# Performance work log

Measured on AMD Instinct MI355X. Metric: run time of the kernel, lower is better.

Reference implementation:

```python
import jax, jax.numpy as jnp
import numpy as np

N, C, K, OUT = 16384, 64, 32, 64
EPS = 1e-5


def knn_idx(x, k):
    # pairwise squared distances, exclude self-loops, take k nearest
    sq = jnp.sum(x * x, axis=1)
    d = sq[:, None] + sq[None, :] - 2.0 * (x @ x.T)  # [N, N]
    n = x.shape[0]
    d = d.at[jnp.arange(n), jnp.arange(n)].set(jnp.inf)
    _, idx = jax.lax.top_k(-d, k)  # [N, k] nearest neighbors
    return idx


def edge_conv(x, idx, W, b, g, beta):
    # EdgeConv: max_j nn(cat([x_i, x_j - x_i])), nn = Lin -> ReLU -> BN
    xi = jnp.broadcast_to(x[:, None, :], (x.shape[0], idx.shape[1], x.shape[1]))
    xj = x[idx]                                   # [N, k, C] gather
    e = jnp.concatenate([xi, xj - xi], axis=-1)   # [N, k, 2C]
    h = jax.nn.relu(e @ W + b)                    # [N, k, H]
    mu = h.mean(axis=(0, 1))
    var = h.var(axis=(0, 1))
    h = (h - mu) * jax.lax.rsqrt(var + EPS) * g + beta  # BN (batch stats)
    return h.max(axis=1)                          # max aggregation over k


def setup_inputs() -> dict:
    key = jax.random.key(0)
    ks = jax.random.split(key, 14)
    s = 0.05
    H = 2 * C
    return {
        "x": jax.random.normal(ks[0], (N, C), dtype=jnp.float32),
        "W1": jax.random.normal(ks[1], (2 * C, H), dtype=jnp.float32) * s,
        "b1": jnp.zeros((H,), jnp.float32),
        "g1": jnp.ones((H,), jnp.float32),
        "beta1": jnp.zeros((H,), jnp.float32),
        "W2": jax.random.normal(ks[2], (2 * H, H), dtype=jnp.float32) * s,
        "b2": jnp.zeros((H,), jnp.float32),
        "g2": jnp.ones((H,), jnp.float32),
        "beta2": jnp.zeros((H,), jnp.float32),
        "lw1": jax.random.normal(ks[3], (H, C), dtype=jnp.float32) * s,
        "lb1": jnp.zeros((C,), jnp.float32),
        "lw2": jax.random.normal(ks[4], (C, OUT), dtype=jnp.float32) * s,
        "lb2": jnp.zeros((OUT,), jnp.float32),
    }


def reference(x, W1, b1, g1, beta1, W2, b2, g2, beta2, lw1, lb1, lw2, lb2):
    idx1 = knn_idx(x, K)
    h1 = edge_conv(x, idx1, W1, b1, g1, beta1)    # [N, 2C]
    idx2 = knn_idx(h1, K)                          # dynamic graph in feature space
    h2 = edge_conv(h1, idx2, W2, b2, g2, beta2)   # [N, 2C]
    h = jax.nn.relu(h2)
    h = jax.nn.relu(h @ lw1 + lb1)                # [N, C]
    return h @ lw2 + lb2                          # [N, OUT]
```

## Files before the change

### kernel.cpp

```cpp
#include <hip/hip_runtime.h>
#include <hip/hip_bf16.h>
#include <math.h>

#define N_PTS 16384
#define KNN_K 32
#define CAP 512
#define HDIM 128
#define TSAMP 4096
#define NSLICE 4
#define LBUF 64

typedef __attribute__((ext_vector_type(8))) short bf16x8;
typedef __attribute__((ext_vector_type(8))) unsigned short us8;
typedef __attribute__((ext_vector_type(4))) float f32x4;

template<int C>
__global__ void sqnorm_np_kernel(const float* __restrict__ feat, float* __restrict__ sq) {
  int r = blockIdx.x * 256 + threadIdx.x;
  if (r >= N_PTS) return;
  const float* xr = feat + (size_t)r * C;
  float acc[8];
  #pragma unroll
  for (int j = 0; j < 8; j++) acc[j] = __fmul_rn(xr[j], xr[j]);
  for (int i = 8; i < C; i += 8) {
    #pragma unroll
    for (int j = 0; j < 8; j++)
      acc[j] = __fadd_rn(acc[j], __fmul_rn(xr[i + j], xr[i + j]));
  }
  float s01 = __fadd_rn(acc[0], acc[1]);
  float s23 = __fadd_rn(acc[2], acc[3]);
  float s45 = __fadd_rn(acc[4], acc[5]);
  float s67 = __fadd_rn(acc[6], acc[7]);
  sq[r] = __fadd_rn(__fadd_rn(s01, s23), __fadd_rn(s45, s67));
}

template<int C>
__global__ void split_swz_kernel(const float* __restrict__ x, unsigned short* __restrict__ hi,
                                 unsigned short* __restrict__ lo) {
  constexpr int CH = C / 8;
  int gid = blockIdx.x * 256 + threadIdx.x;
  int n = gid / CH, c = gid & (CH - 1);
  if (n >= N_PTS) return;
  const float* src = x + (size_t)n * C + c * 8;
  unsigned short h8[8], l8[8];
  #pragma unroll
  for (int j = 0; j < 8; j++) {
    float v = src[j];
    __hip_bfloat16 h = __float2bfloat16(v);
    float hf = __bfloat162float(h);
    __hip_bfloat16 l = __float2bfloat16(v - hf);
    h8[j] = *(unsigned short*)&h;
    l8[j] = *(unsigned short*)&l;
  }
  size_t o = (size_t)n * C + (size_t)(((c ^ (n & (CH - 1)))) * 8);
  *(us8*)(hi + o) = *(const us8*)h8;
  *(us8*)(lo + o) = *(const us8*)l8;
}

template<int C>
__launch_bounds__(512)
__global__ void knn_tau(const unsigned short* __restrict__ xhi,
                        const unsigned short* __restrict__ xlo,
                        const float* __restrict__ sq,
                        float margin, float* __restrict__ tau) {
  constexpr int CH = C / 8, KC = C / 32;
  constexpr int NB = 32 * C * 2;
  constexpr int SEGS = (2 * NB) / 16 / 512;
  __shared__ unsigned char Bs[2 * NB];
  __shared__ float tred[64][65];
  const int t = threadIdx.x;
  const int qbase = blockIdx.x * 64;
  const int wv = t >> 6, lane = t & 63, qd = lane >> 4, l16 = lane & 15;
  const int mi = (wv & 3) * 16, ni = (wv >> 2) * 16;

  bf16x8 ah[KC], al[KC];
  {
    const int arow = qbase + mi + l16;
    const int akey = arow & (CH - 1);
    #pragma unroll
    for (int kc = 0; kc < KC; kc++) {
      size_t o = (size_t)arow * C + (size_t)(((kc * 4 + qd) ^ akey) * 8);
      ah[kc] = *(const bf16x8*)(xhi + o);
      al[kc] = *(const bf16x8*)(xlo + o);
    }
  }
  int qr[4];
  #pragma unroll
  for (int r = 0; r < 4; r++) qr[r] = qbase + mi + qd * 4 + r;
  float t0[4], t1[4];
  #pragma unroll
  for (int r = 0; r < 4; r++) { t0[r] = INFINITY; t1[r] = INFINITY; }

  const int brow = ni + l16;
  const int bkey = brow & (CH - 1);

  us8 regs[SEGS];
  #pragma unroll
  for (int s = 0; s < SEGS; s++) {
    int boff = (t + s * 512) * 16;
    int mtx = boff >= NB;
    int off = boff & (NB - 1);
    regs[s] = *(const us8*)((mtx ? xlo : xhi) + off / 2);
  }
  for (int ti = 0; ti < TSAMP / 32; ti++) {
    __syncthreads();
    #pragma unroll
    for (int s = 0; s < SEGS; s++) {
      int boff = (t + s * 512) * 16;
      int mtx = boff >= NB;
      int off = boff & (NB - 1);
      *(us8*)&Bs[mtx * NB + off] = regs[s];
    }
    __syncthreads();
    if (ti + 1 < TSAMP / 32) {
      #pragma unroll
      for (int s = 0; s < SEGS; s++) {
        int boff = (t + s * 512) * 16;
        int mtx = boff >= NB;
        int off = boff & (NB - 1);
        regs[s] = *(const us8*)((mtx ? xlo : xhi) + (size_t)(ti + 1) * 32 * C + off / 2);
      }
    }
    f32x4 acc = {0.f, 0.f, 0.f, 0.f};
    #pragma unroll
    for (int kc = 0; kc < KC; kc++) {
      size_t bo = (size_t)brow * (2 * C) + (size_t)(((kc * 4 + qd) ^ bkey) * 16);
      bf16x8 bh = *(const bf16x8*)&Bs[bo];
      bf16x8 bl = *(const bf16x8*)&Bs[NB + bo];
      acc = __builtin_amdgcn_mfma_f32_16x16x32_bf16(ah[kc], bh, acc, 0, 0, 0);
      acc = __builtin_amdgcn_mfma_f32_16x16x32_bf16(ah[kc], bl, acc, 0, 0, 0);
      acc = __builtin_amdgcn_mfma_f32_16x16x32_bf16(al[kc], bh, acc, 0, 0, 0);
    }
    const int j = ti * 32 + ni + l16;
    const float sj = sq[j];
    #pragma unroll
    for (int r = 0; r < 4; r++) {
      float d = fmaf(-2.f, acc[r], sj);
      if (d < t1[r] && j != qr[r]) {
        bool lt = d < t0[r];
        t1[r] = lt ? t0[r] : d;
        t0[r] = lt ? d : t0[r];
      }
    }
  }
  const int strm = ni + l16;
  #pragma unroll
  for (int r = 0; r < 4; r++) {
    tred[mi + qd * 4 + r][strm]      = t0[r];
    tred[mi + qd * 4 + r][32 + strm] = t1[r];
  }
  __syncthreads();
  const int tq = t >> 3, i0 = (t & 7) * 8;
  #pragma unroll
  for (int ii = 0; ii < 8; ii++) {
    const int i = i0 + ii;
    const float vi = tred[tq][i];
    int rank = 0;
    for (int m = 0; m < 64; m++) {
      float vm = tred[tq][m];
      rank += (vm < vi || (vm == vi && m < i)) ? 1 : 0;
    }
    if (rank == 32) tau[qbase + tq] = vi + margin;
  }
}

template<int C>
__launch_bounds__(512)
__global__ void knn_filter(const unsigned short* __restrict__ xhi,
                           const unsigned short* __restrict__ xlo,
                           const float* __restrict__ sq,
                           const float* __restrict__ tau,
                           int* __restrict__ cnt, int* __restrict__ list_j,
                           float* __restrict__ list_d) {
  constexpr int CH = C / 8, KC = C / 32;
  constexpr int NB = 32 * C * 2;
  constexpr int SEGS = (2 * NB) / 16 / 512;
  constexpr int JSPAN = N_PTS / NSLICE;
  __shared__ unsigned char Bs[2 * NB];
  __shared__ int   lbj[64 * LBUF];
  __shared__ float lbd[64 * LBUF];
  __shared__ int lcnt[64];
  __shared__ int lbase[64];
  const int t = threadIdx.x;
  const int qbase = blockIdx.x * 64;
  const int jbase = blockIdx.y * JSPAN;
  const int wv = t >> 6, lane = t & 63, qd = lane >> 4, l16 = lane & 15;
  const int mi = (wv & 3) * 16, ni = (wv >> 2) * 16;

  if (t < 64) lcnt[t] = 0;

  bf16x8 ah[KC], al[KC];
  {
    const int arow = qbase + mi + l16;
    const int akey = arow & (CH - 1);
    #pragma unroll
    for (int kc = 0; kc < KC; kc++) {
      size_t o = (size_t)arow * C + (size_t)(((kc * 4 + qd) ^ akey) * 8);
      ah[kc] = *(const bf16x8*)(xhi + o);
      al[kc] = *(const bf16x8*)(xlo + o);
    }
  }
  int lq[4]; float tq[4];
  #pragma unroll
  for (int r = 0; r < 4; r++) {
    lq[r] = mi + qd * 4 + r;
    tq[r] = tau[qbase + lq[r]];
  }
  const int brow = ni + l16;
  const int bkey = brow & (CH - 1);

  us8 regs[SEGS];
  #pragma unroll
  for (int s = 0; s < SEGS; s++) {
    int boff = (t + s * 512) * 16;
    int mtx = boff >= NB;
    int off = boff & (NB - 1);
    regs[s] = *(const us8*)((mtx ? xlo : xhi) + (size_t)jbase * C + off / 2);
  }
  for (int ti = 0; ti < JSPAN / 32; ti++) {
    __syncthreads();
    #pragma unroll
    for (int s = 0; s < SEGS; s++) {
      int boff = (t + s * 512) * 16;
      int mtx = boff >= NB;
      int off = boff & (NB - 1);
      *(us8*)&Bs[mtx * NB + off] = regs[s];
    }
    __syncthreads();
    if (ti + 1 < JSPAN / 32) {
      #pragma unroll
      for (int s = 0; s < SEGS; s++) {
        int boff = (t + s * 512) * 16;
        int mtx = boff >= NB;
        int off = boff & (NB - 1);
        regs[s] = *(const us8*)((mtx ? xlo : xhi) + (size_t)(jbase + (ti + 1) * 32) * C + off / 2);
      }
    }
    f32x4 acc = {0.f, 0.f, 0.f, 0.f};
    #pragma unroll
    for (int kc = 0; kc < KC; kc++) {
      size_t bo = (size_t)brow * (2 * C) + (size_t)(((kc * 4 + qd) ^ bkey) * 16);
      bf16x8 bh = *(const bf16x8*)&Bs[bo];
      bf16x8 bl = *(const bf16x8*)&Bs[NB + bo];
      acc = __builtin_amdgcn_mfma_f32_16x16x32_bf16(ah[kc], bh, acc, 0, 0, 0);
      acc = __builtin_amdgcn_mfma_f32_16x16x32_bf16(ah[kc], bl, acc, 0, 0, 0);
      acc = __builtin_amdgcn_mfma_f32_16x16x32_bf16(al[kc], bh, acc, 0, 0, 0);
    }
    const int j = jbase + ti * 32 + ni + l16;
    const float sj = sq[j];
    #pragma unroll
    for (int r = 0; r < 4; r++) {
      float d = fmaf(-2.f, acc[r], sj);
      if (d <= tq[r] && j != qbase + lq[r]) {
        int pos = atomicAdd(&lcnt[lq[r]], 1);
        if (pos < LBUF) {
          lbj[lq[r] * LBUF + pos] = j;
          lbd[lq[r] * LBUF + pos] = d;
        } else {
          int gp = atomicAdd(&cnt[qbase + lq[r]], 1);
          if (gp < CAP) {
            list_j[(size_t)(qbase + lq[r]) * CAP + gp] = j;
            list_d[(size_t)(qbase + lq[r]) * CAP + gp] = d;
          }
        }
      }
    }
  }
  __syncthreads();
  if (t < 64) {
    int c = lcnt[t]; if (c > LBUF) c = LBUF;
    lcnt[t] = c;
    lbase[t] = atomicAdd(&cnt[qbase + t], c);
  }
  __syncthreads();
  for (int v = t; v < 64 * LBUF; v += 512) {
    int q = v / LBUF, e = v % LBUF;
    if (e < lcnt[q]) {
      int p = lbase[q] + e;
      if (p < CAP) {
        list_j[(size_t)(qbase + q) * CAP + p] = lbj[v];
        list_d[(size_t)(qbase + q) * CAP + p] = lbd[v];
      }
    }
  }
}

__global__ void zero_cnt_kernel(int* __restrict__ cnt) {
  cnt[blockIdx.x * 256 + threadIdx.x] = 0;
}

template<int C>
__launch_bounds__(256)
__global__ void knn_refine_np(const float* __restrict__ feat, const float* __restrict__ sq,
                              const int* __restrict__ cnt, const int* __restrict__ list_j,
                              const float* __restrict__ list_d, float wmarg,
                              int* __restrict__ idx_out) {
  __shared__ float ds[CAP];
  __shared__ int   js[CAP];
  __shared__ int   widx[CAP];
  __shared__ float dnp[CAP];
  __shared__ float xqs[C];
  __shared__ float rows[32 * (C + 1)];
  __shared__ int   jl[32];
  __shared__ float sjl[32];
  __shared__ float cutd;
  __shared__ int   wn;
  const int q = blockIdx.x;
  const int t = threadIdx.x;
  for (int v = t; v < C; v += 256) xqs[v] = feat[(size_t)q * C + v];
  int cq = cnt[q]; if (cq > CAP) cq = CAP;
  const float sqq = sq[q];
  if (t == 0) { wn = 0; cutd = INFINITY; }
  for (int e = t; e < cq; e += 256) {
    js[e] = list_j[(size_t)q * CAP + e];
    ds[e] = list_d[(size_t)q * CAP + e];
  }
  __syncthreads();
  if (cq > KNN_K) {
    for (int e = t; e < cq; e += 256) {
      float d = ds[e]; int j = js[e];
      int rank = 0;
      for (int m = 0; m < cq; m++) {
        float dm = ds[m]; int jm = js[m];
        rank += (dm < d || (dm == d && jm < j)) ? 1 : 0;
      }
      if (rank == KNN_K - 1) cutd = d;
    }
  }
  __syncthreads();
  const float wcut = cutd + wmarg;
  for (int e = t; e < cq; e += 256)
    if (ds[e] <= wcut) { int p = atomicAdd(&wn, 1); widx[p] = e; }
  __syncthreads();
  const int nw = wn;
  for (int base = 0; base < nw; base += 32) {
    const int nc = (nw - base < 32) ? (nw - base) : 32;
    __syncthreads();
    if (t < nc) {
      int j = js[widx[base + t]];
      jl[t] = j;
      sjl[t] = sq[j];
    }
    __syncthreads();
    for (int v = t; v < nc * C; v += 256) {
      int r = v >> ((C == 64) ? 6 : 7);
      int c = v & (C - 1);
      rows[r * (C + 1) + c] = feat[(size_t)jl[r] * C + c];
    }
    __syncthreads();
    if (t < nc) {
      float g = 0.f;
      const float* row = &rows[t * (C + 1)];
      for (int c = 0; c < C; c++) g = fmaf(xqs[c], row[c], g);
      dnp[base + t] = __fsub_rn(__fadd_rn(sqq, sjl[t]), __fmul_rn(2.f, g));
    }
  }
  __syncthreads();
  for (int e = t; e < nw; e += 256) {
    float d = dnp[e]; int j = js[widx[e]];
    int rank = 0;
    for (int m = 0; m < nw; m++) {
      float dm = dnp[m]; int jm = js[widx[m]];
      rank += (dm < d || (dm == d && jm < j)) ? 1 : 0;
    }
    if (rank < KNN_K) idx_out[(size_t)q * KNN_K + rank] = j;
  }
}

template<int C>
__global__ void pq_kernel(const float* __restrict__ feat, const float* __restrict__ W,
                          const float* __restrict__ b, float* __restrict__ P,
                          float* __restrict__ Q) {
  int gid = blockIdx.x * 256 + threadIdx.x;
  int n = gid >> 7, ch = gid & 127;
  const float* xr = feat + (size_t)n * C;
  double p = (double)b[ch], q = 0.0;
  for (int d = 0; d < C; d++) {
    double xv = (double)xr[d];
    p += xv * (double)W[(size_t)d * HDIM + ch];
    q += xv * (double)W[(size_t)(C + d) * HDIM + ch];
  }
  P[gid] = (float)(p - q);
  Q[gid] = (float)q;
}

__global__ void edge_gather2(const float* __restrict__ P, const float* __restrict__ Q,
                             const int* __restrict__ idx, float* __restrict__ hmax,
                             float* __restrict__ hmin, double* __restrict__ stats) {
  __shared__ double red0[256];
  __shared__ double red1[256];
  const int t = threadIdx.x;
  const int ch = t & 127, half = t >> 7;
  const size_t nb = (size_t)blockIdx.x * 16 + (size_t)half * 8;
  double s = 0.0, s2 = 0.0;
  for (int u = 0; u < 8; u++) {
    const size_t n = nb + u;
    double p = (double)P[n * 128 + ch];
    double mx = -1.0e300, mn = 1.0e300;
    for (int k = 0; k < KNN_K; k++) {
      int j = idx[n * KNN_K + k];
      double h = p + (double)Q[(size_t)j * 128 + ch];
      h = h > 0.0 ? h : 0.0;
      mx = h > mx ? h : mx;
      mn = h < mn ? h : mn;
      s += h; s2 += h * h;
    }
    hmax[n * 128 + ch] = (float)mx;
    hmin[n * 128 + ch] = (float)mn;
  }
  red0[t] = s; red1[t] = s2;
  __syncthreads();
  if (t < 128) {
    atomicAdd(&stats[ch],       red0[t] + red0[t + 128]);
    atomicAdd(&stats[128 + ch], red1[t] + red1[t + 128]);
  }
}

__global__ void zero_stats_d(double* __restrict__ stats) {
  stats[threadIdx.x] = 0.0;
}

__global__ void bn_finalize_d(const double* __restrict__ stats, const float* __restrict__ g,
                              const float* __restrict__ beta, double* __restrict__ ss) {
  int ch = threadIdx.x;
  const double inv = 1.0 / ((double)N_PTS * (double)KNN_K);
  double mu = stats[ch] * inv;
  double var = stats[128 + ch] * inv - mu * mu;
  double sc = (double)g[ch] / sqrt(var + 1e-5);
  ss[ch] = sc;
  ss[128 + ch] = (double)beta[ch] - mu * sc;
}

__global__ void ec_out_d(const float* __restrict__ hmax, const float* __restrict__ hmin,
                         const double* __restrict__ ss, float* __restrict__ h_f) {
  size_t i = (size_t)blockIdx.x * 256 + threadIdx.x;
  int ch = (int)(i & 127);
  double sc = ss[ch];
  double v = sc >= 0.0 ? (double)hmax[i] : (double)hmin[i];
  h_f[i] = (float)(v * sc + ss[128 + ch]);
}

__global__ void head1_kernel(const float* __restrict__ h2, const float* __restrict__ lw1,
                             const float* __restrict__ lb1, float* __restrict__ T) {
  int gid = blockIdx.x * 256 + threadIdx.x;
  int n = gid >> 6, hc = gid & 63;
  const float* hr = h2 + (size_t)n * 128;
  double a = (double)lb1[hc];
  for (int d = 0; d < 128; d++) {
    double v = (double)hr[d];
    v = v > 0.0 ? v : 0.0;
    a += v * (double)lw1[(size_t)d * 64 + hc];
  }
  T[gid] = (float)(a > 0.0 ? a : 0.0);
}

__global__ void head2_kernel(const float* __restrict__ T, const float* __restrict__ lw2,
                             const float* __restrict__ lb2, float* __restrict__ out) {
  int gid = blockIdx.x * 256 + threadIdx.x;
  int n = gid >> 6, oc = gid & 63;
  const float* tr = T + (size_t)n * 64;
  double a = (double)lb2[oc];
  for (int d = 0; d < 64; d++) a += (double)tr[d] * (double)lw2[(size_t)d * 64 + oc];
  out[gid] = (float)a;
}

extern "C" void kernel_launch(void* const* d_in, const int* in_sizes, int n_in,
                              void* d_out, int out_size, void* d_ws, size_t ws_size,
                              hipStream_t stream) {
  (void)in_sizes; (void)n_in; (void)out_size; (void)ws_size;
  const float* x     = (const float*)d_in[0];
  const float* W1    = (const float*)d_in[1];
  const float* b1    = (const float*)d_in[2];
  const float* g1    = (const float*)d_in[3];
  const float* beta1 = (const float*)d_in[4];
  const float* W2    = (const float*)d_in[5];
  const float* b2    = (const float*)d_in[6];
  const float* g2    = (const float*)d_in[7];
  const float* beta2 = (const float*)d_in[8];
  const float* lw1   = (const float*)d_in[9];
  const float* lb1   = (const float*)d_in[10];
  const float* lw2   = (const float*)d_in[11];
  const float* lb2   = (const float*)d_in[12];
  float* out = (float*)d_out;

  char* w = (char*)d_ws;
  size_t off = 0;
  auto alloc = [&](size_t bytes) { char* p = w + off; off += (bytes + 255) & ~(size_t)255; return p; };
  float*  sq     = (float*) alloc(N_PTS * 4);
  float*  tau    = (float*) alloc(N_PTS * 4);
  int*    cnt    = (int*)   alloc(N_PTS * 4);
  int*    list_j = (int*)   alloc((size_t)N_PTS * CAP * 4);
  float*  list_d = (float*) alloc((size_t)N_PTS * CAP * 4);
  int*    idx    = (int*)   alloc((size_t)N_PTS * KNN_K * 4);
  unsigned short* xhi = (unsigned short*)alloc((size_t)N_PTS * HDIM * 2);
  unsigned short* xlo = (unsigned short*)alloc((size_t)N_PTS * HDIM * 2);
  float*  P      = (float*) alloc((size_t)N_PTS * HDIM * 4);
  float*  Q      = (float*) alloc((size_t)N_PTS * HDIM * 4);
  float*  hmax   = (float*) alloc((size_t)N_PTS * HDIM * 4);
  float*  hmin   = (float*) alloc((size_t)N_PTS * HDIM * 4);
  double* stats  = (double*)alloc(2 * HDIM * 8);
  double* ss     = (double*)alloc(2 * HDIM * 8);
  float*  h1f    = (float*) alloc((size_t)N_PTS * HDIM * 4);
  float*  h2f    = P;
  float*  T      = Q;

  sqnorm_np_kernel<64><<<N_PTS / 256, 256, 0, stream>>>(x, sq);
  split_swz_kernel<64><<<N_PTS * 8 / 256, 256, 0, stream>>>(x, xhi, xlo);
  knn_tau<64><<<N_PTS / 64, 512, 0, stream>>>(xhi, xlo, sq, 0.05f, tau);
  zero_cnt_kernel<<<N_PTS / 256, 256, 0, stream>>>(cnt);
  knn_filter<64><<<dim3(N_PTS / 64, NSLICE), 512, 0, stream>>>(xhi, xlo, sq, tau, cnt, list_j, list_d);
  knn_refine_np<64><<<N_PTS, 256, 0, stream>>>(x, sq, cnt, list_j, list_d, 0.05f, idx);

  pq_kernel<64><<<N_PTS * 128 / 256, 256, 0, stream>>>(x, W1, b1, P, Q);
  zero_stats_d<<<1, 256, 0, stream>>>(stats);
  edge_gather2<<<N_PTS / 16, 256, 0, stream>>>(P, Q, idx, hmax, hmin, stats);
  bn_finalize_d<<<1, 128, 0, stream>>>(stats, g1, beta1, ss);
  ec_out_d<<<N_PTS * HDIM / 256, 256, 0, stream>>>(hmax, hmin, ss, h1f);

  sqnorm_np_kernel<128><<<N_PTS / 256, 256, 0, stream>>>(h1f, sq);
  split_swz_kernel<128><<<N_PTS * 16 / 256, 256, 0, stream>>>(h1f, xhi, xlo);
  knn_tau<128><<<N_PTS / 64, 512, 0, stream>>>(xhi, xlo, sq, 0.2f, tau);
  zero_cnt_kernel<<<N_PTS / 256, 256, 0, stream>>>(cnt);
  knn_filter<128><<<dim3(N_PTS / 64, NSLICE), 512, 0, stream>>>(xhi, xlo, sq, tau, cnt, list_j, list_d);
  knn_refine_np<128><<<N_PTS, 256, 0, stream>>>(h1f, sq, cnt, list_j, list_d, 0.2f, idx);

  pq_kernel<128><<<N_PTS * 128 / 256, 256, 0, stream>>>(h1f, W2, b2, P, Q);
  zero_stats_d<<<1, 256, 0, stream>>>(stats);
  edge_gather2<<<N_PTS / 16, 256, 0, stream>>>(P, Q, idx, hmax, hmin, stats);
  bn_finalize_d<<<1, 128, 0, stream>>>(stats, g2, beta2, ss);
  ec_out_d<<<N_PTS * HDIM / 256, 256, 0, stream>>>(hmax, hmin, ss, h2f);

  head1_kernel<<<N_PTS * 64 / 256, 256, 0, stream>>>(h2f, lw1, lb1, T);
  head2_kernel<<<N_PTS * 64 / 256, 256, 0, stream>>>(T, lw2, lb2, out);
}
```

Before: 1.331 ms.

## Retile kNN filter to 128x64 tiles with 32x32 MFMA and split hi/lo staging

The kNN distance filter kernel now processes 128 queries per block against 64-point candidate tiles using 32x32x16 bf16 MFMA instead of 16x16x32. The hi and lo bf16 halves of the candidate tile are staged through a single shared buffer in two phases, which halves the shared memory footprint and doubles per-block query reuse of each loaded tile. The aim is to cut global/LDS traffic per distance and raise MFMA efficiency, at the cost of extra barriers per tile, 16 threshold registers per lane, and a smaller per-query local candidate buffer (48 entries) that spills to global atomics more often. Launch bounds now request 4 waves/SIMD occupancy.

```diff
diff --git a/kernel.cpp b/kernel.cpp
--- a/kernel.cpp
+++ b/kernel.cpp
@@ -8,11 +8,12 @@
 #define HDIM 128
 #define TSAMP 4096
 #define NSLICE 4
-#define LBUF 64
+#define LBUF 48
 
 typedef __attribute__((ext_vector_type(8))) short bf16x8;
 typedef __attribute__((ext_vector_type(8))) unsigned short us8;
 typedef __attribute__((ext_vector_type(4))) float f32x4;
+typedef __attribute__((ext_vector_type(16))) float f32x16;
 
 template<int C>
 __global__ void sqnorm_np_kernel(const float* __restrict__ feat, float* __restrict__ sq) {
@@ -165,115 +166,123 @@
 }
 
 template<int C>
-__launch_bounds__(512)
+__launch_bounds__(512, 4)
 __global__ void knn_filter(const unsigned short* __restrict__ xhi,
                            const unsigned short* __restrict__ xlo,
                            const float* __restrict__ sq,
                            const float* __restrict__ tau,
                            int* __restrict__ cnt, int* __restrict__ list_j,
                            float* __restrict__ list_d) {
-  constexpr int CH = C / 8, KC = C / 32;
-  constexpr int NB = 32 * C * 2;
-  constexpr int SEGS = (2 * NB) / 16 / 512;
+  constexpr int CH = C / 8;
+  constexpr int KC = C / 16;
+  constexpr int NB = 64 * C;
+  constexpr int SEGS = (NB * 2) / 16 / 512;
   constexpr int JSPAN = N_PTS / NSLICE;
-  __shared__ unsigned char Bs[2 * NB];
-  __shared__ int   lbj[64 * LBUF];
-  __shared__ float lbd[64 * LBUF];
-  __shared__ int lcnt[64];
-  __shared__ int lbase[64];
+  __shared__ unsigned short Bs[NB];
+  __shared__ int   lbj[128 * LBUF];
+  __shared__ float lbd[128 * LBUF];
+  __shared__ int lcnt[128];
+  __shared__ int lbase[128];
   const int t = threadIdx.x;
-  const int qbase = blockIdx.x * 64;
+  const int qbase = blockIdx.x * 128;
   const int jbase = blockIdx.y * JSPAN;
-  const int wv = t >> 6, lane = t & 63, qd = lane >> 4, l16 = lane & 15;
-  const int mi = (wv & 3) * 16, ni = (wv >> 2) * 16;
-
-  if (t < 64) lcnt[t] = 0;
+  const int wv = t >> 6, lane = t & 63;
+  const int l32 = lane & 31, hk = lane >> 5;
+  const int mi = (wv & 3) * 32, ni = (wv >> 2) * 32;
+
+  if (t < 128) lcnt[t] = 0;
 
   bf16x8 ah[KC], al[KC];
   {
-    const int arow = qbase + mi + l16;
+    const int arow = qbase + mi + l32;
     const int akey = arow & (CH - 1);
     #pragma unroll
-    for (int kc = 0; kc < KC; kc++) {
-      size_t o = (size_t)arow * C + (size_t)(((kc * 4 + qd) ^ akey) * 8);
-      ah[kc] = *(const bf16x8*)(xhi + o);
-      al[kc] = *(const bf16x8*)(xlo + o);
-    }
-  }
-  int lq[4]; float tq[4];
-  #pragma unroll
-  for (int r = 0; r < 4; r++) {
-    lq[r] = mi + qd * 4 + r;
-    tq[r] = tau[qbase + lq[r]];
-  }
-  const int brow = ni + l16;
+    for (int kk = 0; kk < KC; kk++) {
+      size_t o = (size_t)arow * C + (size_t)(((kk * 2 + hk) ^ akey) * 8);
+      ah[kk] = *(const bf16x8*)(xhi + o);
+      al[kk] = *(const bf16x8*)(xlo + o);
+    }
+  }
+  float tq16[16];
+  #pragma unroll
+  for (int r = 0; r < 16; r++) {
+    int lq = mi + (r & 3) + 8 * (r >> 2) + 4 * hk;
+    tq16[r] = tau[qbase + lq];
+  }
+  const int brow = ni + l32;
   const int bkey = brow & (CH - 1);
 
   us8 regs[SEGS];
   #pragma unroll
-  for (int s = 0; s < SEGS; s++) {
-    int boff = (t + s * 512) * 16;
-    int mtx = boff >= NB;
-    int off = boff & (NB - 1);
-    regs[s] = *(const us8*)((mtx ? xlo : xhi) + (size_t)jbase * C + off / 2);
-  }
-  for (int ti = 0; ti < JSPAN / 32; ti++) {
-    __syncthreads();
-    #pragma unroll
-    for (int s = 0; s < SEGS; s++) {
-      int boff = (t + s * 512) * 16;
-      int mtx = boff >= NB;
-      int off = boff & (NB - 1);
-      *(us8*)&Bs[mtx * NB + off] = regs[s];
-    }
-    __syncthreads();
-    if (ti + 1 < JSPAN / 32) {
+  for (int s = 0; s < SEGS; s++)
+    regs[s] = *(const us8*)(xhi + (size_t)jbase * C + (size_t)(t + s * 512) * 8);
+
+  for (int ti = 0; ti < JSPAN / 64; ti++) {
+    const int jb = jbase + ti * 64;
+    __syncthreads();
+    #pragma unroll
+    for (int s = 0; s < SEGS; s++)
+      *(us8*)&Bs[(size_t)(t + s * 512) * 8] = regs[s];
+    __syncthreads();
+    #pragma unroll
+    for (int s = 0; s < SEGS; s++)
+      regs[s] = *(const us8*)(xlo + (size_t)jb * C + (size_t)(t + s * 512) * 8);
+
+    f32x16 acc = {0.f,0.f,0.f,0.f,0.f,0.f,0.f,0.f,0.f,0.f,0.f,0.f,0.f,0.f,0.f,0.f};
+    #pragma unroll
+    for (int kk = 0; kk < KC; kk++) {
+      size_t bo = (size_t)brow * C + (size_t)(((kk * 2 + hk) ^ bkey) * 8);
+      bf16x8 bh = *(const bf16x8*)&Bs[bo];
+      acc = __builtin_amdgcn_mfma_f32_32x32x16_bf16(ah[kk], bh, acc, 0, 0, 0);
+      acc = __builtin_amdgcn_mfma_f32_32x32x16_bf16(al[kk], bh, acc, 0, 0, 0);
+    }
+    __syncthreads();
+    #pragma unroll
+    for (int s = 0; s < SEGS; s++)
+      *(us8*)&Bs[(size_t)(t + s * 512) * 8] = regs[s];
+    __syncthreads();
+    if (ti + 1 < JSPAN / 64) {
       #pragma unroll
-      for (int s = 0; s < SEGS; s++) {
-        int boff = (t + s * 512) * 16;
-        int mtx = boff >= NB;
-        int off = boff & (NB - 1);
-        regs[s] = *(const us8*)((mtx ? xlo : xhi) + (size_t)(jbase + (ti + 1) * 32) * C + off / 2);
-      }
-    }
-    f32x4 acc = {0.f, 0.f, 0.f, 0.f};
-    #pragma unroll
-    for (int kc = 0; kc < KC; kc++) {
-      size_t bo = (size_t)brow * (2 * C) + (size_t)(((kc * 4 + qd) ^ bkey) * 16);
-      bf16x8 bh = *(const bf16x8*)&Bs[bo];
-      bf16x8 bl = *(const bf16x8*)&Bs[NB + bo];
-      acc = __builtin_amdgcn_mfma_f32_16x16x32_bf16(ah[kc], bh, acc, 0, 0, 0);
-      acc = __builtin_amdgcn_mfma_f32_16x16x32_bf16(ah[kc], bl, acc, 0, 0, 0);
-      acc = __builtin_amdgcn_mfma_f32_16x16x32_bf16(al[kc], bh, acc, 0, 0, 0);
-    }
-    const int j = jbase + ti * 32 + ni + l16;
+      for (int s = 0; s < SEGS; s++)
+        regs[s] = *(const us8*)(xhi + (size_t)(jb + 64) * C + (size_t)(t + s * 512) * 8);
+    }
+    #pragma unroll
+    for (int kk = 0; kk < KC; kk++) {
+      size_t bo = (size_t)brow * C + (size_t)(((kk * 2 + hk) ^ bkey) * 8);
+      bf16x8 bl = *(const bf16x8*)&Bs[bo];
+      acc = __builtin_amdgcn_mfma_f32_32x32x16_bf16(ah[kk], bl, acc, 0, 0, 0);
+    }
+    const int j = jb + brow;
     const float sj = sq[j];
     #pragma unroll
-    for (int r = 0; r < 4; r++) {
+    for (int r = 0; r < 16; r++) {
       float d = fmaf(-2.f, acc[r], sj);
-      if (d <= tq[r] && j != qbase + lq[r]) {
-        int pos = atomicAdd(&lcnt[lq[r]], 1);
-        if (pos < LBUF) {
-          lbj[lq[r] * LBUF + pos] = j;
-          lbd[lq[r] * LBUF + pos] = d;
-        } else {
-          int gp = atomicAdd(&cnt[qbase + lq[r]], 1);
-          if (gp < CAP) {
-            list_j[(size_t)(qbase + lq[r]) * CAP + gp] = j;
-            list_d[(size_t)(qbase + lq[r]) * CAP + gp] = d;
+      if (d <= tq16[r]) {
+        int lq = mi + (r & 3) + 8 * (r >> 2) + 4 * hk;
+        if (j != qbase + lq) {
+          int pos = atomicAdd(&lcnt[lq], 1);
+          if (pos < LBUF) {
+            lbj[lq * LBUF + pos] = j;
+            lbd[lq * LBUF + pos] = d;
+          } else {
+            int gp = atomicAdd(&cnt[qbase + lq], 1);
+            if (gp < CAP) {
+              list_j[(size_t)(qbase + lq) * CAP + gp] = j;
+              list_d[(size_t)(qbase + lq) * CAP + gp] = d;
+            }
           }
         }
       }
     }
   }
   __syncthreads();
-  if (t < 64) {
+  if (t < 128) {
     int c = lcnt[t]; if (c > LBUF) c = LBUF;
     lcnt[t] = c;
     lbase[t] = atomicAdd(&cnt[qbase + t], c);
   }
   __syncthreads();
-  for (int v = t; v < 64 * LBUF; v += 512) {
+  for (int v = t; v < 128 * LBUF; v += 512) {
     int q = v / LBUF, e = v % LBUF;
     if (e < lcnt[q]) {
       int p = lbase[q] + e;
@@ -508,7 +517,7 @@
   split_swz_kernel<64><<<N_PTS * 8 / 256, 256, 0, stream>>>(x, xhi, xlo);
   knn_tau<64><<<N_PTS / 64, 512, 0, stream>>>(xhi, xlo, sq, 0.05f, tau);
   zero_cnt_kernel<<<N_PTS / 256, 256, 0, stream>>>(cnt);
-  knn_filter<64><<<dim3(N_PTS / 64, NSLICE), 512, 0, stream>>>(xhi, xlo, sq, tau, cnt, list_j, list_d);
+  knn_filter<64><<<dim3(N_PTS / 128, NSLICE), 512, 0, stream>>>(xhi, xlo, sq, tau, cnt, list_j, list_d);
   knn_refine_np<64><<<N_PTS, 256, 0, stream>>>(x, sq, cnt, list_j, list_d, 0.05f, idx);
 
   pq_kernel<64><<<N_PTS * 128 / 256, 256, 0, stream>>>(x, W1, b1, P, Q);
@@ -521,7 +530,7 @@
   split_swz_kernel<128><<<N_PTS * 16 / 256, 256, 0, stream>>>(h1f, xhi, xlo);
   knn_tau<128><<<N_PTS / 64, 512, 0, stream>>>(xhi, xlo, sq, 0.2f, tau);
   zero_cnt_kernel<<<N_PTS / 256, 256, 0, stream>>>(cnt);
-  knn_filter<128><<<dim3(N_PTS / 64, NSLICE), 512, 0, stream>>>(xhi, xlo, sq, tau, cnt, list_j, list_d);
+  knn_filter<128><<<dim3(N_PTS / 128, NSLICE), 512, 0, stream>>>(xhi, xlo, sq, tau, cnt, list_j, list_d);
   knn_refine_np<128><<<N_PTS, 256, 0, stream>>>(h1f, sq, cnt, list_j, list_d, 0.2f, idx);
 
   pq_kernel<128><<<N_PTS * 128 / 256, 256, 0, stream>>>(h1f, W2, b2, P, Q);
```

New measurement: 1.375 ms. +3.3%, slower.
